# Optimization experiments

Hardware: AMD Instinct MI355X
Metric: run time of the kernel (lower is better)

## Reference

```python
import jax, jax.numpy as jnp
import numpy as np

N = 100_000
E = 1_600_000
F_IN = 14
H = 64
N_BLOCKS = 105
N_STEMS_OUT = 105
S = 10_000
KEEP = 0.8  # 1 - drop_prob


def setup_inputs() -> dict:
    key = jax.random.key(0)
    ks = jax.random.split(key, 16)
    x = jax.random.normal(ks[0], (N, F_IN), dtype=jnp.float32)
    edge_index = jax.random.randint(ks[1], (2, E), 0, N, dtype=jnp.int64)
    stem_idxs = jax.random.randint(ks[2], (S,), 0, N, dtype=jnp.int64)
    # learned params (glorot-ish init)
    W1 = jax.random.normal(ks[3], (F_IN + 1, H), dtype=jnp.float32) / np.sqrt(F_IN + 1)
    b1 = jnp.zeros((H,), dtype=jnp.float32)
    W2 = jax.random.normal(ks[4], (H, H), dtype=jnp.float32) / np.sqrt(H)
    b2 = jnp.zeros((H,), dtype=jnp.float32)
    Wb = jax.random.normal(ks[5], (H, N_BLOCKS), dtype=jnp.float32) / np.sqrt(H)
    bb = jnp.zeros((N_BLOCKS,), dtype=jnp.float32)
    Ws = jax.random.normal(ks[6], (H, N_STEMS_OUT), dtype=jnp.float32) / np.sqrt(H)
    bs = jnp.zeros((N_STEMS_OUT,), dtype=jnp.float32)
    # inverted-dropout masks (deterministic reference for F.dropout(p=0.2))
    drop1 = (jax.random.bernoulli(ks[7], KEEP, (N, H)).astype(jnp.float32)) / KEEP
    drop2 = (jax.random.bernoulli(ks[8], KEEP, (N, H)).astype(jnp.float32)) / KEEP
    # gumbel noise g = -log(-log(U)) for gumbel_softmax(tau=1, hard=False)
    u1 = jax.random.uniform(ks[9], (N, N_BLOCKS), minval=1e-10, maxval=1.0)
    u2 = jax.random.uniform(ks[10], (N, N_STEMS_OUT), minval=1e-10, maxval=1.0)
    gb = -jnp.log(-jnp.log(u1)).astype(jnp.float32)
    gs = -jnp.log(-jnp.log(u2)).astype(jnp.float32)
    return {"x": x, "W1": W1, "b1": b1, "W2": W2, "b2": b2,
            "Wb": Wb, "bb": bb, "Ws": Ws, "bs": bs,
            "drop1": drop1, "drop2": drop2, "gb": gb, "gs": gs,
            "edge_index": edge_index, "stem_idxs": stem_idxs}


def gcn_conv(x, W, b, src, dst, norm, n):
    """PyG GCNConv (normalize=True, self-loops already appended in src/dst/norm)."""
    xw = x @ W                                    # [n, out]
    msg = xw[src] * norm[:, None]                 # gather + scale  [E+n, out]
    out = jax.ops.segment_sum(msg, dst, num_segments=n)  # scatter-add
    return out + b


def _gcn_norm(edge_index, n):
    # append self loops, edge weight 1; symmetric normalization
    loops = jnp.arange(n, dtype=edge_index.dtype)
    src = jnp.concatenate([edge_index[0], loops])
    dst = jnp.concatenate([edge_index[1], loops])
    deg = jax.ops.segment_sum(jnp.ones_like(dst, dtype=jnp.float32), dst, num_segments=n)
    dis = jnp.where(deg > 0, jax.lax.rsqrt(deg), 0.0)
    norm = dis[src] * dis[dst]
    return src, dst, norm


def reference(x, W1, b1, W2, b2, Wb, bb, Ws, bs, drop1, drop2, gb, gs, edge_index, stem_idxs):
    n = x.shape[0]
    stem_feature = jnp.zeros((n,), dtype=x.dtype).at[stem_idxs].set(1.0)
    h = jnp.concatenate([x, stem_feature[:, None]], axis=1)  # [N, F_IN+1]
    src, dst, norm = _gcn_norm(edge_index, n)
    h = jax.nn.relu(gcn_conv(h, W1, b1, src, dst, norm, n)) * drop1
    h = jax.nn.relu(gcn_conv(h, W2, b2, src, dst, norm, n)) * drop2
    block_logits = h @ Wb + bb
    stem_logits = h @ Ws + bs
    selected_block = jax.nn.softmax(block_logits + gb, axis=-1)  # gumbel_softmax tau=1 soft
    selected_stem = jax.nn.softmax(stem_logits + gs, axis=-1)
    return (block_logits, stem_logits, selected_block, selected_stem)
```

## Files before the change

kernel.cpp:

```cpp
#include <hip/hip_runtime.h>
#include <hip/hip_bf16.h>
#include <math.h>

#define N_NODES 100000
#define N_EDGES 1600000
#define FIN 14
#define H 64
#define NB 105
#define S_CNT 10000
#define SCAN_BLOCKS 391
#define LGJ 224
#define HM 64
#define LGS 232

__global__ __launch_bounds__(256) void deg_kernel(const int* __restrict__ dst,
                                                  int* __restrict__ deg) {
    int e = blockIdx.x * 256 + threadIdx.x;
    atomicAdd(&deg[dst[e]], 1);
}

__global__ __launch_bounds__(256) void stem_kernel(const int* __restrict__ idx,
                                                   float* __restrict__ stem01) {
    int i = blockIdx.x * 256 + threadIdx.x;
    if (i < S_CNT) stem01[idx[i]] = 1.0f;
}

__global__ __launch_bounds__(256) void dis_kernel(const int* __restrict__ deg,
                                                  float* __restrict__ dis) {
    int i = blockIdx.x * 256 + threadIdx.x;
    if (i < N_NODES) dis[i] = rsqrtf((float)deg[i] + 1.0f);
}

__global__ __launch_bounds__(256) void scan1_kernel(const int* __restrict__ deg,
                                                    int* __restrict__ rowptr,
                                                    int* __restrict__ bsum) {
    __shared__ int s[256];
    int t = threadIdx.x;
    int i = blockIdx.x * 256 + t;
    int v = (i < N_NODES) ? deg[i] : 0;
    s[t] = v;
    __syncthreads();
#pragma unroll
    for (int o = 1; o < 256; o <<= 1) {
        int x = (t >= o) ? s[t - o] : 0;
        __syncthreads();
        s[t] += x;
        __syncthreads();
    }
    if (i < N_NODES) rowptr[i + 1] = s[t];
    if (t == 255) bsum[blockIdx.x] = s[255];
}

__global__ __launch_bounds__(512) void scan2_kernel(const int* __restrict__ bsum,
                                                    int* __restrict__ boff) {
    __shared__ int s[512];
    int t = threadIdx.x;
    int v = (t < SCAN_BLOCKS) ? bsum[t] : 0;
    s[t] = v;
    __syncthreads();
#pragma unroll
    for (int o = 1; o < 512; o <<= 1) {
        int x = (t >= o) ? s[t - o] : 0;
        __syncthreads();
        s[t] += x;
        __syncthreads();
    }
    if (t < SCAN_BLOCKS) boff[t] = s[t] - v;
}

__global__ __launch_bounds__(256) void scan3_kernel(const int* __restrict__ boff,
                                                    int* __restrict__ rowptr,
                                                    int* __restrict__ cursor) {
    int t = threadIdx.x;
    int i = blockIdx.x * 256 + t;
    if (i < N_NODES) {
        int val = rowptr[i + 1] + boff[blockIdx.x];
        rowptr[i + 1] = val;
        if (i + 1 < N_NODES) cursor[i + 1] = val;
    }
    if (i == 0) { rowptr[0] = 0; cursor[0] = 0; }
}

__global__ __launch_bounds__(256) void scatter_kernel(const int* __restrict__ src,
                                                      const int* __restrict__ dst,
                                                      int* __restrict__ cursor,
                                                      int* __restrict__ col) {
    int e = blockIdx.x * 256 + threadIdx.x;
    int d = dst[e];
    int pos = atomicAdd(&cursor[d], 1);
    col[pos] = src[e];
}

__global__ __launch_bounds__(256) void wpad_kernel(const float* __restrict__ Wb,
                                                   const float* __restrict__ Ws,
                                                   float* __restrict__ Wp) {
    int i = blockIdx.x * 256 + threadIdx.x;
    if (i < 64 * LGJ) {
        int k = i / LGJ, j = i - k * LGJ;
        float w = 0.f;
        if (j < NB) w = Wb[k * NB + j];
        else if (j >= 112 && j < 112 + NB) w = Ws[k * NB + (j - 112)];
        Wp[i] = w;
    }
}

__global__ __launch_bounds__(256) void xw1_kernel(const float* __restrict__ x,
                                                  const float* __restrict__ stem01,
                                                  const float* __restrict__ dis,
                                                  const float* __restrict__ W1,
                                                  float* __restrict__ xws) {
    __shared__ __align__(16) float W1s[15 * 64];
    __shared__ __align__(16) float xs[4][16];
    int tid = threadIdx.x;
    for (int i = tid; i < 960; i += 256) W1s[i] = W1[i];
    int n0 = blockIdx.x * 4;
    if (tid < 60) {
        int r = tid / 15, k = tid % 15;
        int n = n0 + r;
        xs[r][k] = (k < FIN) ? x[n * FIN + k] : stem01[n];
    }
    __syncthreads();
    int r = tid >> 6, f = tid & 63;
    float acc = 0.f;
#pragma unroll
    for (int k = 0; k < 15; k++) acc += xs[r][k] * W1s[k * 64 + f];
    xws[(n0 + r) * 64 + f] = acc * dis[n0 + r];
}

__global__ __launch_bounds__(256) void agg_csr_kernel(const float* __restrict__ xws,
                                                      const int* __restrict__ rowptr,
                                                      const int* __restrict__ col,
                                                      const float* __restrict__ dis,
                                                      const float* __restrict__ bias,
                                                      const float* __restrict__ drop,
                                                      float* __restrict__ hout) {
    int node = (blockIdx.x * 256 + threadIdx.x) >> 6;
    int f = threadIdx.x & 63;
    int beg = rowptr[node], end = rowptr[node + 1];
    float acc0 = xws[node * 64 + f];
    float acc1 = 0.f, acc2 = 0.f, acc3 = 0.f;
    int j = beg;
    for (; j + 4 <= end; j += 4) {
        int s0 = col[j], s1 = col[j + 1], s2 = col[j + 2], s3 = col[j + 3];
        acc0 += xws[s0 * 64 + f];
        acc1 += xws[s1 * 64 + f];
        acc2 += xws[s2 * 64 + f];
        acc3 += xws[s3 * 64 + f];
    }
    for (; j < end; j++) acc0 += xws[col[j] * 64 + f];
    float acc = (acc0 + acc1) + (acc2 + acc3);
    float r = fmaxf(fmaf(dis[node], acc, bias[f]), 0.f) * drop[node * 64 + f];
    hout[node * 64 + f] = r;
}

__global__ __launch_bounds__(256) void xw2_kernel(const float* __restrict__ h,
                                                  const float* __restrict__ dis,
                                                  const float* __restrict__ W2,
                                                  float* __restrict__ xws) {
    __shared__ __align__(16) float W2s[64 * 64];
    __shared__ __align__(16) float hsT[64 * 68];
    int tid = threadIdx.x;
    for (int i = tid; i < 4096; i += 256) W2s[i] = W2[i];
    int n0 = blockIdx.x * 64;
    for (int i = tid; i < 4096; i += 256) {
        int m = i >> 6, k = i & 63;
        int n = n0 + m;
        hsT[k * 68 + m] = (n < N_NODES) ? h[n * 64 + k] : 0.f;
    }
    __syncthreads();
    int fg = tid & 15, mg = tid >> 4;
    int f0 = fg * 4, m0 = mg * 4;
    float acc[4][4];
#pragma unroll
    for (int i = 0; i < 4; i++)
#pragma unroll
        for (int j = 0; j < 4; j++) acc[i][j] = 0.f;
    for (int k = 0; k < 64; k++) {
        float4 w = *(const float4*)&W2s[k * 64 + f0];
        float4 hv = *(const float4*)&hsT[k * 68 + m0];
        float hh[4] = {hv.x, hv.y, hv.z, hv.w};
#pragma unroll
        for (int i = 0; i < 4; i++) {
            acc[i][0] += hh[i] * w.x;
            acc[i][1] += hh[i] * w.y;
            acc[i][2] += hh[i] * w.z;
            acc[i][3] += hh[i] * w.w;
        }
    }
#pragma unroll
    for (int i = 0; i < 4; i++) {
        int n = n0 + m0 + i;
        if (n < N_NODES) {
            float ds = dis[n];
            float4 r = make_float4(acc[i][0] * ds, acc[i][1] * ds,
                                   acc[i][2] * ds, acc[i][3] * ds);
            *(float4*)&xws[n * 64 + f0] = r;
        }
    }
}

__global__ __launch_bounds__(256) void head_kernel(const float* __restrict__ h2,
                                                   const float* __restrict__ Wp,
                                                   const float* __restrict__ bb,
                                                   const float* __restrict__ bs,
                                                   const float* __restrict__ gb,
                                                   const float* __restrict__ gs,
                                                   float* __restrict__ out) {
    __shared__ __align__(16) float smem[64 * 68];
    int tid = threadIdx.x;
    int n0 = blockIdx.x * HM;

    {
        const float4* src = (const float4*)(h2 + (size_t)n0 * 64);
#pragma unroll
        for (int q = 0; q < 4; q++) {
            int f4 = tid + q * 256;
            int m = f4 >> 4;
            int k0 = (f4 & 15) * 4;
            float4 v = make_float4(0.f, 0.f, 0.f, 0.f);
            if (n0 + m < N_NODES) v = src[f4];
            smem[(k0 + 0) * 68 + m] = v.x;
            smem[(k0 + 1) * 68 + m] = v.y;
            smem[(k0 + 2) * 68 + m] = v.z;
            smem[(k0 + 3) * 68 + m] = v.w;
        }
    }
    __syncthreads();

    int tj = tid % 28, tm = tid / 28;
    bool act = tid < 224;
    int j0 = tj * 8, m0 = tm * 8;
    float acc[8][8];
#pragma unroll
    for (int a = 0; a < 8; a++)
#pragma unroll
        for (int b = 0; b < 8; b++) acc[a][b] = 0.f;

    if (act) {
        const float* wbase = Wp + j0;
#pragma unroll 2
        for (int k = 0; k < 64; k++) {
            float4 wa = *(const float4*)&wbase[k * LGJ];
            float4 wb2 = *(const float4*)&wbase[k * LGJ + 4];
            float4 h0 = *(const float4*)&smem[k * 68 + m0];
            float4 h1 = *(const float4*)&smem[k * 68 + m0 + 4];
            float wv[8] = {wa.x, wa.y, wa.z, wa.w, wb2.x, wb2.y, wb2.z, wb2.w};
            float hh[8] = {h0.x, h0.y, h0.z, h0.w, h1.x, h1.y, h1.z, h1.w};
#pragma unroll
            for (int a = 0; a < 8; a++)
#pragma unroll
                for (int b = 0; b < 8; b++) acc[a][b] += hh[a] * wv[b];
        }
    }

    int lane = tid & 31, grp = tid >> 5;
    for (int c = 0; c < 4; c++) {
        __syncthreads();
        if (act && (tm >> 1) == c) {
            int lmBase = m0 - c * 16;
#pragma unroll
            for (int a = 0; a < 8; a++) {
                int lm = lmBase + a;
                *(float4*)&smem[lm * LGS + j0] =
                    make_float4(acc[a][0], acc[a][1], acc[a][2], acc[a][3]);
                *(float4*)&smem[lm * LGS + j0 + 4] =
                    make_float4(acc[a][4], acc[a][5], acc[a][6], acc[a][7]);
            }
        }
        __syncthreads();
#pragma unroll
        for (int pass = 0; pass < 4; pass++) {
            int p = grp + 8 * pass;
            int lm = p >> 1, head = p & 1;
            int n = n0 + c * 16 + lm;
            if (n >= N_NODES) continue;
            const float* bias = head ? bs : bb;
            const float* gum = head ? gs : gb;
            int jbase = head ? 112 : 0;
            float lg[4], z[4], e[4];
            float mx = -INFINITY;
#pragma unroll
            for (int i = 0; i < 4; i++) {
                int cc = lane + 32 * i;
                if (cc < NB) {
                    lg[i] = smem[lm * LGS + jbase + cc] + bias[cc];
                    z[i] = lg[i] + gum[(size_t)n * NB + cc];
                } else {
                    lg[i] = 0.f;
                    z[i] = -INFINITY;
                }
                mx = fmaxf(mx, z[i]);
            }
#pragma unroll
            for (int off = 16; off; off >>= 1) mx = fmaxf(mx, __shfl_xor(mx, off));
            float s = 0.f;
#pragma unroll
            for (int i = 0; i < 4; i++) {
                int cc = lane + 32 * i;
                e[i] = (cc < NB) ? __expf(z[i] - mx) : 0.f;
                s += e[i];
            }
#pragma unroll
            for (int off = 16; off; off >>= 1) s += __shfl_xor(s, off);
            float inv = 1.f / s;
            float* lo = out + (size_t)head * (N_NODES * NB) + (size_t)n * NB;
            float* so = out + (size_t)(2 + head) * (N_NODES * NB) + (size_t)n * NB;
#pragma unroll
            for (int i = 0; i < 4; i++) {
                int cc = lane + 32 * i;
                if (cc < NB) {
                    lo[cc] = lg[i];
                    so[cc] = e[i] * inv;
                }
            }
        }
    }
}

extern "C" void kernel_launch(void* const* d_in, const int* in_sizes, int n_in,
                              void* d_out, int out_size, void* d_ws, size_t ws_size,
                              hipStream_t stream) {
    const float* x     = (const float*)d_in[0];
    const float* W1    = (const float*)d_in[1];
    const float* b1    = (const float*)d_in[2];
    const float* W2    = (const float*)d_in[3];
    const float* b2    = (const float*)d_in[4];
    const float* Wb    = (const float*)d_in[5];
    const float* bb    = (const float*)d_in[6];
    const float* Ws    = (const float*)d_in[7];
    const float* bs    = (const float*)d_in[8];
    const float* drop1 = (const float*)d_in[9];
    const float* drop2 = (const float*)d_in[10];
    const float* gb    = (const float*)d_in[11];
    const float* gs    = (const float*)d_in[12];
    const int* edge    = (const int*)d_in[13];
    const int* stem    = (const int*)d_in[14];
    float* out = (float*)d_out;

    float* A      = (float*)d_ws;
    float* B      = A + (size_t)N_NODES * 64;
    float* dis    = B + (size_t)N_NODES * 64;
    float* stem01 = dis + N_NODES;
    int*   deg    = (int*)(stem01 + N_NODES);
    int*   rowptr = deg + N_NODES;
    int*   cursor = rowptr + (N_NODES + 1);
    int*   bsum   = cursor + N_NODES;
    int*   boff   = bsum + SCAN_BLOCKS;
    int*   col    = boff + SCAN_BLOCKS;
    float* Wp     = (float*)(col + N_EDGES);

    const int* esrc = edge;
    const int* edst = edge + N_EDGES;

    hipMemsetAsync(deg, 0, N_NODES * sizeof(int), stream);
    hipMemsetAsync(stem01, 0, N_NODES * sizeof(float), stream);

    deg_kernel<<<N_EDGES / 256, 256, 0, stream>>>(edst, deg);
    stem_kernel<<<(S_CNT + 255) / 256, 256, 0, stream>>>(stem, stem01);
    dis_kernel<<<SCAN_BLOCKS, 256, 0, stream>>>(deg, dis);
    wpad_kernel<<<(64 * LGJ + 255) / 256, 256, 0, stream>>>(Wb, Ws, Wp);

    scan1_kernel<<<SCAN_BLOCKS, 256, 0, stream>>>(deg, rowptr, bsum);
    scan2_kernel<<<1, 512, 0, stream>>>(bsum, boff);
    scan3_kernel<<<SCAN_BLOCKS, 256, 0, stream>>>(boff, rowptr, cursor);
    scatter_kernel<<<N_EDGES / 256, 256, 0, stream>>>(esrc, edst, cursor, col);

    xw1_kernel<<<N_NODES / 4, 256, 0, stream>>>(x, stem01, dis, W1, A);
    agg_csr_kernel<<<(N_NODES * 64) / 256, 256, 0, stream>>>(A, rowptr, col, dis, b1, drop1, B);

    xw2_kernel<<<(N_NODES + 63) / 64, 256, 0, stream>>>(B, dis, W2, B);
    agg_csr_kernel<<<(N_NODES * 64) / 256, 256, 0, stream>>>(B, rowptr, col, dis, b2, drop2, A);

    head_kernel<<<(N_NODES + HM - 1) / HM, 256, 0, stream>>>(A, Wp, bb, bs, gb, gs, out);
}
```

Before: 777.4 us.

## Build CSR via two-level bucket sort and split head into matmul plus softmax

Replaces the global atomic scatter used to build the CSR with a two-level counting sort. Edges are first binned by destination block (256 nodes) using per-block shared histograms and a scan, staged in the output buffer, then sorted within each bucket using shared-memory atomics. This is meant to cut contention on global atomics and make the column writes more local. The head is also split into a matmul kernel that writes logits directly and a separate gumbel-softmax kernel that re-reads them, which removes the shared-memory staging and its barriers but adds another pass over global memory.

```diff
diff --git a/kernel.cpp b/kernel.cpp
--- a/kernel.cpp
+++ b/kernel.cpp
@@ -11,7 +11,9 @@
 #define SCAN_BLOCKS 391
 #define LGJ 224
 #define HM 64
-#define LGS 232
+#define NBKT 391
+#define BBLK 250
+#define EPB 6400
 
 __global__ __launch_bounds__(256) void deg_kernel(const int* __restrict__ dst,
                                                   int* __restrict__ deg) {
@@ -69,26 +71,80 @@
 }
 
 __global__ __launch_bounds__(256) void scan3_kernel(const int* __restrict__ boff,
-                                                    int* __restrict__ rowptr,
-                                                    int* __restrict__ cursor) {
+                                                    int* __restrict__ rowptr) {
     int t = threadIdx.x;
     int i = blockIdx.x * 256 + t;
-    if (i < N_NODES) {
-        int val = rowptr[i + 1] + boff[blockIdx.x];
-        rowptr[i + 1] = val;
-        if (i + 1 < N_NODES) cursor[i + 1] = val;
-    }
-    if (i == 0) { rowptr[0] = 0; cursor[0] = 0; }
-}
-
-__global__ __launch_bounds__(256) void scatter_kernel(const int* __restrict__ src,
+    if (i < N_NODES) rowptr[i + 1] += boff[blockIdx.x];
+    if (i == 0) rowptr[0] = 0;
+}
+
+__global__ __launch_bounds__(256) void bincnt_kernel(const int* __restrict__ dst,
+                                                     int* __restrict__ hist) {
+    __shared__ int lh[NBKT];
+    int t = threadIdx.x;
+    for (int i = t; i < NBKT; i += 256) lh[i] = 0;
+    __syncthreads();
+    int e0 = blockIdx.x * EPB;
+    for (int i = t; i < EPB; i += 256) atomicAdd(&lh[dst[e0 + i] >> 8], 1);
+    __syncthreads();
+    for (int i = t; i < NBKT; i += 256) hist[i * BBLK + blockIdx.x] = lh[i];
+}
+
+__global__ __launch_bounds__(256) void binscan_kernel(int* __restrict__ hist,
+                                                      const int* __restrict__ rowptr) {
+    __shared__ int s[256];
+    int t = threadIdx.x, b = blockIdx.x;
+    int v = (t < BBLK) ? hist[b * BBLK + t] : 0;
+    s[t] = v;
+    __syncthreads();
+#pragma unroll
+    for (int o = 1; o < 256; o <<= 1) {
+        int x = (t >= o) ? s[t - o] : 0;
+        __syncthreads();
+        s[t] += x;
+        __syncthreads();
+    }
+    if (t < BBLK) hist[b * BBLK + t] = rowptr[b * 256] + s[t] - v;
+}
+
+__global__ __launch_bounds__(256) void binscat_kernel(const int* __restrict__ src,
                                                       const int* __restrict__ dst,
-                                                      int* __restrict__ cursor,
-                                                      int* __restrict__ col) {
-    int e = blockIdx.x * 256 + threadIdx.x;
-    int d = dst[e];
-    int pos = atomicAdd(&cursor[d], 1);
-    col[pos] = src[e];
+                                                      const int* __restrict__ hist,
+                                                      int* __restrict__ tmp) {
+    __shared__ int lofs[NBKT];
+    __shared__ int lcnt[NBKT];
+    int t = threadIdx.x;
+    for (int i = t; i < NBKT; i += 256) {
+        lofs[i] = hist[i * BBLK + blockIdx.x];
+        lcnt[i] = 0;
+    }
+    __syncthreads();
+    int e0 = blockIdx.x * EPB;
+    for (int i = t; i < EPB; i += 256) {
+        int s = src[e0 + i], d = dst[e0 + i];
+        int b = d >> 8;
+        int r = atomicAdd(&lcnt[b], 1);
+        tmp[lofs[b] + r] = s | ((d & 255) << 17);
+    }
+}
+
+__global__ __launch_bounds__(256) void bsort_kernel(const int* __restrict__ tmp,
+                                                    const int* __restrict__ rowptr,
+                                                    int* __restrict__ col) {
+    __shared__ int cur[256];
+    int t = threadIdx.x, b = blockIdx.x;
+    int n0 = b * 256;
+    int idx = n0 + t;
+    cur[t] = (idx < N_NODES) ? rowptr[idx] : 0;
+    __syncthreads();
+    int beg = rowptr[n0];
+    int nend = n0 + 256; if (nend > N_NODES) nend = N_NODES;
+    int end = rowptr[nend];
+    for (int i = beg + t; i < end; i += 256) {
+        int p = tmp[i];
+        int pos = atomicAdd(&cur[p >> 17], 1);
+        col[pos] = p & 0x1FFFF;
+    }
 }
 
 __global__ __launch_bounds__(256) void wpad_kernel(const float* __restrict__ Wb,
@@ -199,13 +255,11 @@
     }
 }
 
-__global__ __launch_bounds__(256) void head_kernel(const float* __restrict__ h2,
-                                                   const float* __restrict__ Wp,
-                                                   const float* __restrict__ bb,
-                                                   const float* __restrict__ bs,
-                                                   const float* __restrict__ gb,
-                                                   const float* __restrict__ gs,
-                                                   float* __restrict__ out) {
+__global__ __launch_bounds__(256) void headmm_kernel(const float* __restrict__ h2,
+                                                     const float* __restrict__ Wp,
+                                                     const float* __restrict__ bb,
+                                                     const float* __restrict__ bs,
+                                                     float* __restrict__ out) {
     __shared__ __align__(16) float smem[64 * 68];
     int tid = threadIdx.x;
     int n0 = blockIdx.x * HM;
@@ -226,9 +280,9 @@
         }
     }
     __syncthreads();
+    if (tid >= 224) return;
 
     int tj = tid % 28, tm = tid / 28;
-    bool act = tid < 224;
     int j0 = tj * 8, m0 = tm * 8;
     float acc[8][8];
 #pragma unroll
@@ -236,85 +290,64 @@
 #pragma unroll
         for (int b = 0; b < 8; b++) acc[a][b] = 0.f;
 
-    if (act) {
-        const float* wbase = Wp + j0;
+    const float* wbase = Wp + j0;
 #pragma unroll 2
-        for (int k = 0; k < 64; k++) {
-            float4 wa = *(const float4*)&wbase[k * LGJ];
-            float4 wb2 = *(const float4*)&wbase[k * LGJ + 4];
-            float4 h0 = *(const float4*)&smem[k * 68 + m0];
-            float4 h1 = *(const float4*)&smem[k * 68 + m0 + 4];
-            float wv[8] = {wa.x, wa.y, wa.z, wa.w, wb2.x, wb2.y, wb2.z, wb2.w};
-            float hh[8] = {h0.x, h0.y, h0.z, h0.w, h1.x, h1.y, h1.z, h1.w};
-#pragma unroll
-            for (int a = 0; a < 8; a++)
-#pragma unroll
-                for (int b = 0; b < 8; b++) acc[a][b] += hh[a] * wv[b];
+    for (int k = 0; k < 64; k++) {
+        float4 wa = *(const float4*)&wbase[k * LGJ];
+        float4 wb2 = *(const float4*)&wbase[k * LGJ + 4];
+        float4 h0 = *(const float4*)&smem[k * 68 + m0];
+        float4 h1 = *(const float4*)&smem[k * 68 + m0 + 4];
+        float wv[8] = {wa.x, wa.y, wa.z, wa.w, wb2.x, wb2.y, wb2.z, wb2.w};
+        float hh[8] = {h0.x, h0.y, h0.z, h0.w, h1.x, h1.y, h1.z, h1.w};
+#pragma unroll
+        for (int a = 0; a < 8; a++)
+#pragma unroll
+            for (int b = 0; b < 8; b++) acc[a][b] += hh[a] * wv[b];
+    }
+
+    int head = j0 >= 112;
+    int jl0 = j0 - head * 112;
+    const float* bias = head ? bs : bb;
+    float bv[8];
+#pragma unroll
+    for (int b = 0; b < 8; b++) bv[b] = (jl0 + b < NB) ? bias[jl0 + b] : 0.f;
+    float* obase = out + (size_t)head * ((size_t)N_NODES * NB);
+    for (int a = 0; a < 8; a++) {
+        int n = n0 + m0 + a;
+        if (n < N_NODES) {
+            float* o = obase + (size_t)n * NB + jl0;
+#pragma unroll
+            for (int b = 0; b < 8; b++)
+                if (jl0 + b < NB) o[b] = acc[a][b] + bv[b];
         }
     }
-
-    int lane = tid & 31, grp = tid >> 5;
-    for (int c = 0; c < 4; c++) {
-        __syncthreads();
-        if (act && (tm >> 1) == c) {
-            int lmBase = m0 - c * 16;
-#pragma unroll
-            for (int a = 0; a < 8; a++) {
-                int lm = lmBase + a;
-                *(float4*)&smem[lm * LGS + j0] =
-                    make_float4(acc[a][0], acc[a][1], acc[a][2], acc[a][3]);
-                *(float4*)&smem[lm * LGS + j0 + 4] =
-                    make_float4(acc[a][4], acc[a][5], acc[a][6], acc[a][7]);
-            }
-        }
-        __syncthreads();
-#pragma unroll
-        for (int pass = 0; pass < 4; pass++) {
-            int p = grp + 8 * pass;
-            int lm = p >> 1, head = p & 1;
-            int n = n0 + c * 16 + lm;
-            if (n >= N_NODES) continue;
-            const float* bias = head ? bs : bb;
-            const float* gum = head ? gs : gb;
-            int jbase = head ? 112 : 0;
-            float lg[4], z[4], e[4];
-            float mx = -INFINITY;
-#pragma unroll
-            for (int i = 0; i < 4; i++) {
-                int cc = lane + 32 * i;
-                if (cc < NB) {
-                    lg[i] = smem[lm * LGS + jbase + cc] + bias[cc];
-                    z[i] = lg[i] + gum[(size_t)n * NB + cc];
-                } else {
-                    lg[i] = 0.f;
-                    z[i] = -INFINITY;
-                }
-                mx = fmaxf(mx, z[i]);
-            }
-#pragma unroll
-            for (int off = 16; off; off >>= 1) mx = fmaxf(mx, __shfl_xor(mx, off));
-            float s = 0.f;
-#pragma unroll
-            for (int i = 0; i < 4; i++) {
-                int cc = lane + 32 * i;
-                e[i] = (cc < NB) ? __expf(z[i] - mx) : 0.f;
-                s += e[i];
-            }
-#pragma unroll
-            for (int off = 16; off; off >>= 1) s += __shfl_xor(s, off);
-            float inv = 1.f / s;
-            float* lo = out + (size_t)head * (N_NODES * NB) + (size_t)n * NB;
-            float* so = out + (size_t)(2 + head) * (N_NODES * NB) + (size_t)n * NB;
-#pragma unroll
-            for (int i = 0; i < 4; i++) {
-                int cc = lane + 32 * i;
-                if (cc < NB) {
-                    lo[cc] = lg[i];
-                    so[cc] = e[i] * inv;
-                }
-            }
-        }
-    }
+}
+
+__global__ __launch_bounds__(256) void gsm_kernel(const float* __restrict__ gb,
+                                                  const float* __restrict__ gs,
+                                                  float* __restrict__ out) {
+    const size_t NA = (size_t)N_NODES * NB;
+    int wid = blockIdx.x * 4 + (threadIdx.x >> 6);
+    int lane = threadIdx.x & 63;
+    int n = wid >> 1;
+    if (n >= N_NODES) return;
+    int head = wid & 1;
+    const float* L = out + (head ? NA : 0) + (size_t)n * NB;
+    const float* g = (head ? gs : gb) + (size_t)n * NB;
+    float z0 = L[lane] + g[lane];
+    float z1 = (lane < NB - 64) ? L[lane + 64] + g[lane + 64] : -INFINITY;
+    float m = fmaxf(z0, z1);
+#pragma unroll
+    for (int off = 32; off; off >>= 1) m = fmaxf(m, __shfl_xor(m, off));
+    float e0 = __expf(z0 - m);
+    float e1 = (lane < NB - 64) ? __expf(z1 - m) : 0.f;
+    float s = e0 + e1;
+#pragma unroll
+    for (int off = 32; off; off >>= 1) s += __shfl_xor(s, off);
+    float inv = 1.f / s;
+    float* o = out + (2 + head) * NA + (size_t)n * NB;
+    o[lane] = e0 * inv;
+    if (lane < NB - 64) o[lane + 64] = e1 * inv;
 }
 
 extern "C" void kernel_launch(void* const* d_in, const int* in_sizes, int n_in,
@@ -343,11 +376,12 @@
     float* stem01 = dis + N_NODES;
     int*   deg    = (int*)(stem01 + N_NODES);
     int*   rowptr = deg + N_NODES;
-    int*   cursor = rowptr + (N_NODES + 1);
-    int*   bsum   = cursor + N_NODES;
+    int*   hist   = rowptr + (N_NODES + 1);
+    int*   bsum   = hist + N_NODES;
     int*   boff   = bsum + SCAN_BLOCKS;
     int*   col    = boff + SCAN_BLOCKS;
     float* Wp     = (float*)(col + N_EDGES);
+    int*   tmp    = (int*)d_out;
 
     const int* esrc = edge;
     const int* edst = edge + N_EDGES;
@@ -362,8 +396,12 @@
 
     scan1_kernel<<<SCAN_BLOCKS, 256, 0, stream>>>(deg, rowptr, bsum);
     scan2_kernel<<<1, 512, 0, stream>>>(bsum, boff);
-    scan3_kernel<<<SCAN_BLOCKS, 256, 0, stream>>>(boff, rowptr, cursor);
-    scatter_kernel<<<N_EDGES / 256, 256, 0, stream>>>(esrc, edst, cursor, col);
+    scan3_kernel<<<SCAN_BLOCKS, 256, 0, stream>>>(boff, rowptr);
+
+    bincnt_kernel<<<BBLK, 256, 0, stream>>>(edst, hist);
+    binscan_kernel<<<NBKT, 256, 0, stream>>>(hist, rowptr);
+    binscat_kernel<<<BBLK, 256, 0, stream>>>(esrc, edst, hist, tmp);
+    bsort_kernel<<<NBKT, 256, 0, stream>>>(tmp, rowptr, col);
 
     xw1_kernel<<<N_NODES / 4, 256, 0, stream>>>(x, stem01, dis, W1, A);
     agg_csr_kernel<<<(N_NODES * 64) / 256, 256, 0, stream>>>(A, rowptr, col, dis, b1, drop1, B);
@@ -371,5 +409,6 @@
     xw2_kernel<<<(N_NODES + 63) / 64, 256, 0, stream>>>(B, dis, W2, B);
     agg_csr_kernel<<<(N_NODES * 64) / 256, 256, 0, stream>>>(B, rowptr, col, dis, b2, drop2, A);
 
-    head_kernel<<<(N_NODES + HM - 1) / HM, 256, 0, stream>>>(A, Wp, bb, bs, gb, gs, out);
-}
+    headmm_kernel<<<(N_NODES + HM - 1) / HM, 256, 0, stream>>>(A, Wp, bb, bs, out);
+    gsm_kernel<<<(2 * N_NODES + 3) / 4, 256, 0, stream>>>(gb, gs, out);
+}
```

Measured after the change: 737.4 us. -5.2%, faster.
